# Performance work log

Measured on AMD Instinct MI355X. Metric: run time of the kernel, lower is better.

## Reference

```python
import jax, jax.numpy as jnp
import numpy as np

INPUT_DIM = 1024
HIDDEN = [4096, 4096, 4096]
OUTPUT_DIM = 1024


def _cplx(a):
    # a: float32 array with leading axis 2 = (real, imag)
    return (a[0] + 1j * a[1]).astype(jnp.complex64)


def setup_inputs() -> dict:
    key = jax.random.key(0)
    ks = list(jax.random.split(key, 16))
    O = [INPUT_DIM] + HIDDEN[:-1] + [OUTPUT_DIM]  # O[0], O[1], O[2], O[3]
    I = HIDDEN  # I[1..3]
    inp = {"x": jax.random.normal(ks[0], (2, INPUT_DIM), dtype=jnp.float32)}
    for l in range(3):
        Il, Ol, Oprev = I[l], O[l + 1], O[l]
        w_std = 1.0 / np.sqrt(Il)
        c_std = 1.0 / np.sqrt(2 * Oprev)
        inp[f"W{l+1}"] = (jax.random.normal(ks[1 + 4 * l], (2, Ol, Il), dtype=jnp.float32) * w_std)
        inp[f"b{l+1}"] = jnp.zeros((2, Ol), dtype=jnp.float32)
        inp[f"G{l+1}"] = (jax.random.normal(ks[2 + 4 * l], (2, Il, Oprev), dtype=jnp.float32) * c_std)
        inp[f"s{l+1}"] = jnp.ones((Il,), dtype=jnp.float32)
    return inp


def _rbf_layer(y, W, b, G, s):
    # y: (O_prev,) complex; G: (I, O_prev) complex; W: (O, I); s: (I,) float
    diff = y[None, :] - G                                   # (I, O_prev)
    dist_sq = jnp.sum(diff.real ** 2 + diff.imag ** 2, axis=-1)  # (I,)
    phi = jnp.exp(-dist_sq / (2.0 * s))                     # (I,) real Gaussian kernel
    return W @ phi.astype(W.dtype) + b                      # (O,) complex


def reference(x, W1, b1, G1, s1, W2, b2, G2, s2, W3, b3, G3, s3):
    y = _cplx(x)
    for (W, b, G, s) in ((W1, b1, G1, s1), (W2, b2, G2, s2), (W3, b3, G3, s3)):
        y = _rbf_layer(y, _cplx(W), _cplx(b), _cplx(G), s)
    # return real/imag stacked as a real float32 array, shape (2, OUTPUT_DIM)
    return jnp.stack([y.real, y.imag]).astype(jnp.float32)
```

## Files before the change

### kernel.cpp

```cpp
#include <hip/hip_runtime.h>


#define INPUT_DIM 1024
#define HID 4096
#define OUT_DIM 1024

__device__ __forceinline__ float wave_reduce_sum(float v) {
#pragma unroll
    for (int off = 32; off > 0; off >>= 1) v += __shfl_down(v, off, 64);
    return v;
}

__device__ __forceinline__ void block_reduce2(float& a, float& b, float* sred) {
    a = wave_reduce_sum(a);
    b = wave_reduce_sum(b);
    const int lane = threadIdx.x & 63;
    const int wave = threadIdx.x >> 6;
    if (lane == 0) { sred[wave] = a; sred[4 + wave] = b; }
    __syncthreads();
    if (threadIdx.x == 0) {
        a = sred[0] + sred[1] + sred[2] + sred[3];
        b = sred[4] + sred[5] + sred[6] + sred[7];
    }
}

__global__ __launch_bounds__(256) void rbf_phi(
        const float* __restrict__ Gre, const float* __restrict__ Gim,
        const float* __restrict__ yre, const float* __restrict__ yim,
        const float* __restrict__ s, float* __restrict__ phi, int Oprev) {
    extern __shared__ float sm[];
    float* sy_re = sm;
    float* sy_im = sm + Oprev;
    float* sred  = sm + 2 * Oprev;

    for (int j = threadIdx.x * 4; j < Oprev; j += blockDim.x * 4) {
        *(float4*)(sy_re + j) = *(const float4*)(yre + j);
        *(float4*)(sy_im + j) = *(const float4*)(yim + j);
    }
    __syncthreads();

    const int i = blockIdx.x;
    const float* gre = Gre + (size_t)i * Oprev;
    const float* gim = Gim + (size_t)i * Oprev;

    float acc = 0.f, acc2 = 0.f;
    for (int j = threadIdx.x * 4; j < Oprev; j += blockDim.x * 4) {
        float4 gr = *(const float4*)(gre + j);
        float4 gi = *(const float4*)(gim + j);
        float4 yr = *(const float4*)(sy_re + j);
        float4 yi = *(const float4*)(sy_im + j);
        float dr, di;
        dr = yr.x - gr.x; di = yi.x - gi.x; acc  += dr * dr + di * di;
        dr = yr.y - gr.y; di = yi.y - gi.y; acc2 += dr * dr + di * di;
        dr = yr.z - gr.z; di = yi.z - gi.z; acc  += dr * dr + di * di;
        dr = yr.w - gr.w; di = yi.w - gi.w; acc2 += dr * dr + di * di;
    }
    block_reduce2(acc, acc2, sred);
    if (threadIdx.x == 0) {
        float d = acc + acc2;
        phi[i] = expf(-d / (2.0f * s[i]));
    }
}

__global__ __launch_bounds__(256) void rbf_w(
        const float* __restrict__ Wre, const float* __restrict__ Wim,
        const float* __restrict__ bre, const float* __restrict__ bim,
        const float* __restrict__ phi,
        float* __restrict__ out_re, float* __restrict__ out_im, int I) {
    extern __shared__ float sm[];
    float* sphi = sm;
    float* sred = sm + I;

    for (int j = threadIdx.x * 4; j < I; j += blockDim.x * 4)
        *(float4*)(sphi + j) = *(const float4*)(phi + j);
    __syncthreads();

    const int o = blockIdx.x;
    const float* wre = Wre + (size_t)o * I;
    const float* wim = Wim + (size_t)o * I;

    float ar = 0.f, ai = 0.f;
    for (int j = threadIdx.x * 4; j < I; j += blockDim.x * 4) {
        float4 wr = *(const float4*)(wre + j);
        float4 wi = *(const float4*)(wim + j);
        float4 p  = *(const float4*)(sphi + j);
        ar += wr.x * p.x + wr.y * p.y + wr.z * p.z + wr.w * p.w;
        ai += wi.x * p.x + wi.y * p.y + wi.z * p.z + wi.w * p.w;
    }
    block_reduce2(ar, ai, sred);
    if (threadIdx.x == 0) {
        out_re[o] = ar + bre[o];
        out_im[o] = ai + bim[o];
    }
}

extern "C" void kernel_launch(void* const* d_in, const int* in_sizes, int n_in,
                              void* d_out, int out_size, void* d_ws, size_t ws_size,
                              hipStream_t stream) {
    const float* x  = (const float*)d_in[0];
    const float* W1 = (const float*)d_in[1];
    const float* b1 = (const float*)d_in[2];
    const float* G1 = (const float*)d_in[3];
    const float* s1 = (const float*)d_in[4];
    const float* W2 = (const float*)d_in[5];
    const float* b2 = (const float*)d_in[6];
    const float* G2 = (const float*)d_in[7];
    const float* s2 = (const float*)d_in[8];
    const float* W3 = (const float*)d_in[9];
    const float* b3 = (const float*)d_in[10];
    const float* G3 = (const float*)d_in[11];
    const float* s3 = (const float*)d_in[12];
    float* out = (float*)d_out;

    float* ws  = (float*)d_ws;
    float* phi = ws;
    float* yre = ws + 4096;
    float* yim = ws + 8192;

    const int TB = 256;
    {
        const float* Gre = G1, *Gim = G1 + (size_t)HID * INPUT_DIM;
        rbf_phi<<<HID, TB, (2 * INPUT_DIM + 8) * sizeof(float), stream>>>(
            Gre, Gim, x, x + INPUT_DIM, s1, phi, INPUT_DIM);
        const float* Wre = W1, *Wim = W1 + (size_t)HID * HID;
        rbf_w<<<HID, TB, (HID + 8) * sizeof(float), stream>>>(
            Wre, Wim, b1, b1 + HID, phi, yre, yim, HID);
    }
    {
        const float* Gre = G2, *Gim = G2 + (size_t)HID * HID;
        rbf_phi<<<HID, TB, (2 * HID + 8) * sizeof(float), stream>>>(
            Gre, Gim, yre, yim, s2, phi, HID);
        const float* Wre = W2, *Wim = W2 + (size_t)HID * HID;
        rbf_w<<<HID, TB, (HID + 8) * sizeof(float), stream>>>(
            Wre, Wim, b2, b2 + HID, phi, yre, yim, HID);
    }
    {
        const float* Gre = G3, *Gim = G3 + (size_t)HID * HID;
        rbf_phi<<<HID, TB, (2 * HID + 8) * sizeof(float), stream>>>(
            Gre, Gim, yre, yim, s3, phi, HID);
        const float* Wre = W3, *Wim = W3 + (size_t)OUT_DIM * HID;
        rbf_w<<<OUT_DIM, TB, (HID + 8) * sizeof(float), stream>>>(
            Wre, Wim, b3, b3 + OUT_DIM, phi, out, out + OUT_DIM, HID);
    }
}
```

Baseline: 137.7 us.

## Map one wavefront per row with unrolled templated loads, dropping shared memory

Result: faster. 119.3 us (-13.4%).

```diff
diff --git a/kernel.cpp b/kernel.cpp
--- a/kernel.cpp
+++ b/kernel.cpp
@@ -1,96 +1,86 @@
 #include <hip/hip_runtime.h>
 
 
-#define INPUT_DIM 1024
-#define HID 4096
-#define OUT_DIM 1024
+#define D0 1024
+#define H  4096
 
-__device__ __forceinline__ float wave_reduce_sum(float v) {
+__device__ __forceinline__ float wave_sum(float v) {
 #pragma unroll
     for (int off = 32; off > 0; off >>= 1) v += __shfl_down(v, off, 64);
     return v;
 }
 
-__device__ __forceinline__ void block_reduce2(float& a, float& b, float* sred) {
-    a = wave_reduce_sum(a);
-    b = wave_reduce_sum(b);
+template <int COLS, int ROWS>
+__global__ __launch_bounds__(256) void phi_k(
+        const float* __restrict__ G,
+        const float* __restrict__ yre, const float* __restrict__ yim,
+        const float* __restrict__ sv, float* __restrict__ phi) {
     const int lane = threadIdx.x & 63;
-    const int wave = threadIdx.x >> 6;
-    if (lane == 0) { sred[wave] = a; sred[4 + wave] = b; }
-    __syncthreads();
-    if (threadIdx.x == 0) {
-        a = sred[0] + sred[1] + sred[2] + sred[3];
-        b = sred[4] + sred[5] + sred[6] + sred[7];
+    const int row = (blockIdx.x * 256 + threadIdx.x) >> 6;
+    const float* gre = G + (size_t)row * COLS;
+    const float* gim = gre + (size_t)ROWS * COLS;
+
+    constexpr int NIT = COLS / 256;
+    float acc = 0.f;
+#pragma unroll
+    for (int it0 = 0; it0 < NIT; it0 += 4) {
+        float4 gr[4], gi[4], yr[4], yi[4];
+#pragma unroll
+        for (int u = 0; u < 4; ++u) {
+            const int j = lane * 4 + (it0 + u) * 256;
+            gr[u] = *(const float4*)(gre + j);
+            gi[u] = *(const float4*)(gim + j);
+            yr[u] = *(const float4*)(yre + j);
+            yi[u] = *(const float4*)(yim + j);
+        }
+#pragma unroll
+        for (int u = 0; u < 4; ++u) {
+            float dr, di;
+            dr = yr[u].x - gr[u].x; di = yi[u].x - gi[u].x; acc += dr * dr + di * di;
+            dr = yr[u].y - gr[u].y; di = yi[u].y - gi[u].y; acc += dr * dr + di * di;
+            dr = yr[u].z - gr[u].z; di = yi[u].z - gi[u].z; acc += dr * dr + di * di;
+            dr = yr[u].w - gr[u].w; di = yi[u].w - gi[u].w; acc += dr * dr + di * di;
+        }
     }
+    acc = wave_sum(acc);
+    if (lane == 0) phi[row] = expf(-acc / (2.0f * sv[row]));
 }
 
-__global__ __launch_bounds__(256) void rbf_phi(
-        const float* __restrict__ Gre, const float* __restrict__ Gim,
-        const float* __restrict__ yre, const float* __restrict__ yim,
-        const float* __restrict__ s, float* __restrict__ phi, int Oprev) {
-    extern __shared__ float sm[];
-    float* sy_re = sm;
-    float* sy_im = sm + Oprev;
-    float* sred  = sm + 2 * Oprev;
+template <int COLS, int ROWS>
+__global__ __launch_bounds__(256) void w_k(
+        const float* __restrict__ W, const float* __restrict__ bias,
+        const float* __restrict__ phi,
+        float* __restrict__ ore, float* __restrict__ oim) {
+    const int lane = threadIdx.x & 63;
+    const int row = (blockIdx.x * 256 + threadIdx.x) >> 6;
+    const float* wre = W + (size_t)row * COLS;
+    const float* wim = wre + (size_t)ROWS * COLS;
 
-    for (int j = threadIdx.x * 4; j < Oprev; j += blockDim.x * 4) {
-        *(float4*)(sy_re + j) = *(const float4*)(yre + j);
-        *(float4*)(sy_im + j) = *(const float4*)(yim + j);
+    constexpr int NIT = COLS / 256;
+    float ar = 0.f, ai = 0.f;
+#pragma unroll
+    for (int it0 = 0; it0 < NIT; it0 += 4) {
+        float4 wr[4], wi[4], p[4];
+#pragma unroll
+        for (int u = 0; u < 4; ++u) {
+            const int j = lane * 4 + (it0 + u) * 256;
+            wr[u] = *(const float4*)(wre + j);
+            wi[u] = *(const float4*)(wim + j);
+            p[u]  = *(const float4*)(phi + j);
+        }
+#pragma unroll
+        for (int u = 0; u < 4; ++u) {
+            ar += wr[u].x * p[u].x + wr[u].y * p[u].y
+                + wr[u].z * p[u].z + wr[u].w * p[u].w;
+            ai += wi[u].x * p[u].x + wi[u].y * p[u].y
+                + wi[u].z * p[u].z + wi[u].w * p[u].w;
+        }
     }
-    __syncthreads();
-
-    const int i = blockIdx.x;
-    const float* gre = Gre + (size_t)i * Oprev;
-    const float* gim = Gim + (size_t)i * Oprev;
-
-    float acc = 0.f, acc2 = 0.f;
-    for (int j = threadIdx.x * 4; j < Oprev; j += blockDim.x * 4) {
-        float4 gr = *(const float4*)(gre + j);
-        float4 gi = *(const float4*)(gim + j);
-        float4 yr = *(const float4*)(sy_re + j);
-        float4 yi = *(const float4*)(sy_im + j);
-        float dr, di;
-        dr = yr.x - gr.x; di = yi.x - gi.x; acc  += dr * dr + di * di;
-        dr = yr.y - gr.y; di = yi.y - gi.y; acc2 += dr * dr + di * di;
-        dr = yr.z - gr.z; di = yi.z - gi.z; acc  += dr * dr + di * di;
-        dr = yr.w - gr.w; di = yi.w - gi.w; acc2 += dr * dr + di * di;
-    }
-    block_reduce2(acc, acc2, sred);
-    if (threadIdx.x == 0) {
-        float d = acc + acc2;
-        phi[i] = expf(-d / (2.0f * s[i]));
-    }
-}
-
-__global__ __launch_bounds__(256) void rbf_w(
-        const float* __restrict__ Wre, const float* __restrict__ Wim,
-        const float* __restrict__ bre, const float* __restrict__ bim,
-        const float* __restrict__ phi,
-        float* __restrict__ out_re, float* __restrict__ out_im, int I) {
-    extern __shared__ float sm[];
-    float* sphi = sm;
-    float* sred = sm + I;
-
-    for (int j = threadIdx.x * 4; j < I; j += blockDim.x * 4)
-        *(float4*)(sphi + j) = *(const float4*)(phi + j);
-    __syncthreads();
-
-    const int o = blockIdx.x;
-    const float* wre = Wre + (size_t)o * I;
-    const float* wim = Wim + (size_t)o * I;
-
-    float ar = 0.f, ai = 0.f;
-    for (int j = threadIdx.x * 4; j < I; j += blockDim.x * 4) {
-        float4 wr = *(const float4*)(wre + j);
-        float4 wi = *(const float4*)(wim + j);
-        float4 p  = *(const float4*)(sphi + j);
-        ar += wr.x * p.x + wr.y * p.y + wr.z * p.z + wr.w * p.w;
-        ai += wi.x * p.x + wi.y * p.y + wi.z * p.z + wi.w * p.w;
-    }
-    block_reduce2(ar, ai, sred);
-    if (threadIdx.x == 0) {
-        out_re[o] = ar + bre[o];
-        out_im[o] = ai + bim[o];
+    ar = wave_sum(ar);
+    ai = wave_sum(ai);
+    if (lane == 0) {
+        ore[row] = ar + bias[row];
+        oim[row] = ai + bias[ROWS + row];
     }
 }
 
@@ -114,32 +104,13 @@
 
     float* ws  = (float*)d_ws;
     float* phi = ws;
-    float* yre = ws + 4096;
-    float* yim = ws + 8192;
+    float* yre = ws + H;
+    float* yim = ws + 2 * H;
 
-    const int TB = 256;
-    {
-        const float* Gre = G1, *Gim = G1 + (size_t)HID * INPUT_DIM;
-        rbf_phi<<<HID, TB, (2 * INPUT_DIM + 8) * sizeof(float), stream>>>(
-            Gre, Gim, x, x + INPUT_DIM, s1, phi, INPUT_DIM);
-        const float* Wre = W1, *Wim = W1 + (size_t)HID * HID;
-        rbf_w<<<HID, TB, (HID + 8) * sizeof(float), stream>>>(
-            Wre, Wim, b1, b1 + HID, phi, yre, yim, HID);
-    }
-    {
-        const float* Gre = G2, *Gim = G2 + (size_t)HID * HID;
-        rbf_phi<<<HID, TB, (2 * HID + 8) * sizeof(float), stream>>>(
-            Gre, Gim, yre, yim, s2, phi, HID);
-        const float* Wre = W2, *Wim = W2 + (size_t)HID * HID;
-        rbf_w<<<HID, TB, (HID + 8) * sizeof(float), stream>>>(
-            Wre, Wim, b2, b2 + HID, phi, yre, yim, HID);
-    }
-    {
-        const float* Gre = G3, *Gim = G3 + (size_t)HID * HID;
-        rbf_phi<<<HID, TB, (2 * HID + 8) * sizeof(float), stream>>>(
-            Gre, Gim, yre, yim, s3, phi, HID);
-        const float* Wre = W3, *Wim = W3 + (size_t)OUT_DIM * HID;
-        rbf_w<<<OUT_DIM, TB, (HID + 8) * sizeof(float), stream>>>(
-            Wre, Wim, b3, b3 + OUT_DIM, phi, out, out + OUT_DIM, HID);
-    }
+    phi_k<D0, H><<<H / 4, 256, 0, stream>>>(G1, x, x + D0, s1, phi);
+    w_k<H, H><<<H / 4, 256, 0, stream>>>(W1, b1, phi, yre, yim);
+    phi_k<H, H><<<H / 4, 256, 0, stream>>>(G2, yre, yim, s2, phi);
+    w_k<H, H><<<H / 4, 256, 0, stream>>>(W2, b2, phi, yre, yim);
+    phi_k<H, H><<<H / 4, 256, 0, stream>>>(G3, yre, yim, s3, phi);
+    w_k<H, D0><<<D0 / 4, 256, 0, stream>>>(W3, b3, phi, out, out + D0);
 }
```
